# Optimization experiments

Hardware: AMD Instinct MI355X
Metric: run time of the kernel (lower is better)

Reference implementation:

```python
import jax, jax.numpy as jnp
import numpy as np

B, S, T, D_IN = 32, 64, 30, 500  # batch, outer seq, LSTM time steps, LSTM input size
L = 64  # stacked LSTM layers, hidden_size = 1


def setup_inputs() -> dict:
    key = jax.random.key(0)
    ks = jax.random.split(key, 9)
    s = 0.2  # param scale ~ uniform(-1,1) stddev regime of torch init (1/sqrt(hidden)=1)
    return {
        "x": jax.random.normal(ks[0], (B, S, T * D_IN), jnp.float32),
        "w_ih0": jax.random.normal(ks[1], (4, D_IN), jnp.float32) * s,
        "w_hh0": jax.random.normal(ks[2], (4, 1), jnp.float32) * s,
        "b_ih0": jax.random.normal(ks[3], (4,), jnp.float32) * s,
        "b_hh0": jax.random.normal(ks[4], (4,), jnp.float32) * s,
        "w_ih": jax.random.normal(ks[5], (L - 1, 4, 1), jnp.float32) * s,
        "w_hh": jax.random.normal(ks[6], (L - 1, 4, 1), jnp.float32) * s,
        "b_ih": jax.random.normal(ks[7], (L - 1, 4), jnp.float32) * s,
        "b_hh": jax.random.normal(ks[8], (L - 1, 4), jnp.float32) * s,
    }


def _scan_layer(pre, whh):
    """Run one hidden-width-1 LSTM layer. pre: (T, N, 4) input-side gate preacts
    (incl. both biases); whh: (4,) recurrent weights. Returns hidden stream (T, N)."""
    N = pre.shape[1]
    z = jnp.zeros((N,), pre.dtype)

    def cell(carry, g_in):
        h, c = carry
        g = g_in + h[:, None] * whh  # (N, 4), torch gate order i,f,g,o
        i = jax.nn.sigmoid(g[:, 0])
        f = jax.nn.sigmoid(g[:, 1])
        gg = jnp.tanh(g[:, 2])
        o = jax.nn.sigmoid(g[:, 3])
        c = f * c + i * gg
        h = o * jnp.tanh(c)
        return (h, c), h

    _, hs = jax.lax.scan(cell, (z, z), pre)
    return hs  # (T, N)


def reference(x, w_ih0, w_hh0, b_ih0, b_hh0, w_ih, w_hh, b_ih, b_hh):
    b, s, d = x.shape
    xf = jnp.flip(x, -1).reshape(b * s, T, D_IN)  # (N, T, 500)
    # layer 0: precompute input contribution for all timesteps (the only GEMM)
    pre0 = jnp.einsum('ntd,gd->tng', xf, w_ih0) + b_ih0 + b_hh0  # (T, N, 4)
    hs = _scan_layer(pre0, w_hh0[:, 0])  # (T, N)

    # layers 1..63: scalar-input LSTMs, scanned over the layer axis
    def layer_step(seq, params):
        wih, whh, bias = params  # (4,), (4,), (4,)
        pre = seq[:, :, None] * wih + bias  # (T, N, 4)
        return _scan_layer(pre, whh), None

    hs, _ = jax.lax.scan(layer_step, hs, (w_ih[:, :, 0], w_hh[:, :, 0], b_ih + b_hh))
    return hs.transpose(1, 0).reshape(b, s, T)  # (B, S, 30)
```

## Files before the change

### kernel.cpp

```cpp
#include <hip/hip_runtime.h>

#define NSEQ 2048
#define TT 30
#define DIN 500
#define NLAYER 64

__device__ __forceinline__ float fexp(float x) {
    return __builtin_amdgcn_exp2f(x * 1.4426950408889634f);
}
__device__ __forceinline__ float fsigmoid(float x) {
    return __builtin_amdgcn_rcpf(1.0f + fexp(-x));
}
__device__ __forceinline__ float ftanh_(float x) {
    return fmaf(-2.0f, __builtin_amdgcn_rcpf(1.0f + fexp(2.0f * x)), 1.0f);
}
__device__ __forceinline__ float rdlane(float v, int l) {
    return __builtin_bit_cast(float, __builtin_amdgcn_readlane(__builtin_bit_cast(int, v), l));
}
template <int CTRL>
__device__ __forceinline__ float dppmv(float v) {
    return __builtin_bit_cast(float, __builtin_amdgcn_update_dpp(
        0, __builtin_bit_cast(int, v), CTRL, 0xF, 0xF, false));
}
#define DPP_XOR1 0xB1
#define DPP_XOR2 0x4E
#define DPP_ROR4 0x124
#define DPP_ROR8 0x128
#define DPP_SHR1 0x138

__device__ __forceinline__ float dot4rev(const float4 xv, const float4 wv, float acc) {
    acc = fmaf(xv.x, wv.w, acc);
    acc = fmaf(xv.y, wv.z, acc);
    acc = fmaf(xv.z, wv.y, acc);
    acc = fmaf(xv.w, wv.x, acc);
    return acc;
}

__global__ __launch_bounds__(256, 2) void fused_lstm(
    const float* __restrict__ x,
    const float* __restrict__ w_ih0,
    const float* __restrict__ w_hh0,
    const float* __restrict__ b_ih0,
    const float* __restrict__ b_hh0,
    const float* __restrict__ w_ih,
    const float* __restrict__ w_hh,
    const float* __restrict__ b_ih,
    const float* __restrict__ b_hh,
    float* __restrict__ out)
{
    __shared__ float pre[4][TT * 4];

    const int tid  = threadIdx.x;
    const int lane = tid & 63;
    const int w    = tid >> 6;
    const int n    = blockIdx.x * 4 + w;
    const int s    = lane & 15;
    const int g    = lane >> 4;
    float* __restrict__ prew = pre[w];

    const float4* __restrict__ w4 = (const float4*)w_ih0;
    const float4 z4 = make_float4(0.f, 0.f, 0.f, 0.f);
    float4 wk[8];
#pragma unroll
    for (int k = 0; k < 8; ++k) {
        const int j = k * 16 + s;
        wk[k] = (j < 125) ? w4[g * 125 + (124 - j)] : z4;
    }

    const float4* __restrict__ xq = (const float4*)(x + (size_t)n * (TT * DIN));
    auto xload = [&](int t, float4 (&b)[8]) {
        const float4* __restrict__ p = xq + (TT - 1 - t) * 125;
#pragma unroll
        for (int k = 0; k < 8; ++k) {
            const int j = k * 16 + s;
            b[k] = p[(j < 125) ? j : 124];
        }
    };
    auto compute = [&](const float4 (&b)[8], int t) {
        float a = 0.f;
#pragma unroll
        for (int k = 0; k < 8; ++k) a = dot4rev(b[k], wk[k], a);
        a += dppmv<DPP_XOR1>(a);
        a += dppmv<DPP_XOR2>(a);
        a += dppmv<DPP_ROR4>(a);
        a += dppmv<DPP_ROR8>(a);
        if (s == 0) prew[t * 4 + g] = a;
    };

    float4 A[8], B[8];
    xload(0, A);
#pragma unroll
    for (int t = 0; t < TT; t += 2) {
        xload(t + 1, B);
        compute(A, t);
        if (t + 2 < TT) xload(t + 2, A);
        compute(B, t + 1);
    }
    asm volatile("s_waitcnt lgkmcnt(0)" ::: "memory");

    float wih0 = 0.f, wih1 = 0.f, wih2 = 0.f, wih3 = 0.f;
    float whh0, whh1, whh2, whh3;
    float bia0 = 0.f, bia1 = 0.f, bia2 = 0.f, bia3 = 0.f;
    if (lane == 0) {
        whh0 = w_hh0[0]; whh1 = w_hh0[1]; whh2 = w_hh0[2]; whh3 = w_hh0[3];
    } else {
        const int l = lane - 1;
        wih0 = w_ih[l * 4 + 0]; wih1 = w_ih[l * 4 + 1];
        wih2 = w_ih[l * 4 + 2]; wih3 = w_ih[l * 4 + 3];
        whh0 = w_hh[l * 4 + 0]; whh1 = w_hh[l * 4 + 1];
        whh2 = w_hh[l * 4 + 2]; whh3 = w_hh[l * 4 + 3];
        bia0 = b_ih[l * 4 + 0] + b_hh[l * 4 + 0];
        bia1 = b_ih[l * 4 + 1] + b_hh[l * 4 + 1];
        bia2 = b_ih[l * 4 + 2] + b_hh[l * 4 + 2];
        bia3 = b_ih[l * 4 + 3] + b_hh[l * 4 + 3];
    }
    float pg0 = 0.f, pg1 = 0.f, pg2 = 0.f, pg3 = 0.f;
    if (lane < TT) {
        const float4 q = *(const float4*)&prew[lane * 4];
        pg0 = q.x + b_ih0[0] + b_hh0[0];
        pg1 = q.y + b_ih0[1] + b_hh0[1];
        pg2 = q.z + b_ih0[2] + b_hh0[2];
        pg3 = q.w + b_ih0[3] + b_hh0[3];
    }

    float h = 0.f, c = 0.f;
    for (int k = 0; k < NLAYER + TT - 1; ++k) {
        const float h_in = dppmv<DPP_SHR1>(h);
        const int t = k - lane;
        const bool active = (t >= 0) && (t < TT);

        float g0, g1, g2, g3;
        if (lane == 0) {
            g0 = g1 = g2 = g3 = 0.f;
        } else {
            g0 = fmaf(h_in, wih0, bia0);
            g1 = fmaf(h_in, wih1, bia1);
            g2 = fmaf(h_in, wih2, bia2);
            g3 = fmaf(h_in, wih3, bia3);
        }
        if (k < TT) {
            const float p0 = rdlane(pg0, k);
            const float p1 = rdlane(pg1, k);
            const float p2 = rdlane(pg2, k);
            const float p3 = rdlane(pg3, k);
            if (lane == 0) { g0 = p0; g1 = p1; g2 = p2; g3 = p3; }
        }
        g0 = fmaf(h, whh0, g0);
        g1 = fmaf(h, whh1, g1);
        g2 = fmaf(h, whh2, g2);
        g3 = fmaf(h, whh3, g3);

        const float ig = fsigmoid(g0);
        const float fg = fsigmoid(g1);
        const float gg = ftanh_(g2);
        const float og = fsigmoid(g3);
        const float cn = fmaf(fg, c, ig * gg);
        const float hn = og * ftanh_(cn);

        if (active) { c = cn; h = hn; }
        if (lane == 63 && active) out[(size_t)n * TT + t] = hn;
    }
}

extern "C" void kernel_launch(void* const* d_in, const int* in_sizes, int n_in,
                              void* d_out, int out_size, void* d_ws, size_t ws_size,
                              hipStream_t stream) {
    const float* x     = (const float*)d_in[0];
    const float* w_ih0 = (const float*)d_in[1];
    const float* w_hh0 = (const float*)d_in[2];
    const float* b_ih0 = (const float*)d_in[3];
    const float* b_hh0 = (const float*)d_in[4];
    const float* w_ih  = (const float*)d_in[5];
    const float* w_hh  = (const float*)d_in[6];
    const float* b_ih  = (const float*)d_in[7];
    const float* b_hh  = (const float*)d_in[8];
    float* out = (float*)d_out;

    fused_lstm<<<NSEQ / 4, 256, 0, stream>>>(x, w_ih0, w_hh0, b_ih0, b_hh0,
                                             w_ih, w_hh, b_ih, b_hh, out);
}
```

Baseline: 42.80 us.

## Compute all four gates per lane group over distinct timesteps to reuse x loads

Reorganizes the layer-0 input projection so each 16-lane group processes a different timestep and accumulates all four gate dot products, loading each x row once per wave instead of once per gate group. All w_ih0 gate weights are held in registers. Small parameter loads are also vectorized and hoisted before the GEMM. This raises register pressure substantially and wastes two timestep slots in the final round.

Measured after the change: 42.11 us. Within noise of the previous version (-1.6%).

```diff
diff --git a/kernel.cpp b/kernel.cpp
--- a/kernel.cpp
+++ b/kernel.cpp
@@ -34,6 +34,13 @@
     acc = fmaf(xv.z, wv.y, acc);
     acc = fmaf(xv.w, wv.x, acc);
     return acc;
+}
+__device__ __forceinline__ float red16(float a) {
+    a += dppmv<DPP_XOR1>(a);
+    a += dppmv<DPP_XOR2>(a);
+    a += dppmv<DPP_ROR4>(a);
+    a += dppmv<DPP_ROR8>(a);
+    return a;
 }
 
 __global__ __launch_bounds__(256, 2) void fused_lstm(
@@ -58,69 +65,86 @@
     const int g    = lane >> 4;
     float* __restrict__ prew = pre[w];
 
+    const int l = (lane == 0) ? 0 : (lane - 1);
+    float4 wihv  = *(const float4*)(w_ih + l * 4);
+    float4 whhv  = *(const float4*)(w_hh + l * 4);
+    float4 bihv  = *(const float4*)(b_ih + l * 4);
+    float4 bhhv  = *(const float4*)(b_hh + l * 4);
+    float4 whh0v = *(const float4*)(w_hh0);
+    float4 bi0v  = *(const float4*)(b_ih0);
+    float4 bh0v  = *(const float4*)(b_hh0);
+    __builtin_amdgcn_sched_barrier(0);
+
     const float4* __restrict__ w4 = (const float4*)w_ih0;
     const float4 z4 = make_float4(0.f, 0.f, 0.f, 0.f);
-    float4 wk[8];
-#pragma unroll
-    for (int k = 0; k < 8; ++k) {
-        const int j = k * 16 + s;
-        wk[k] = (j < 125) ? w4[g * 125 + (124 - j)] : z4;
+    float4 wk[4][8];
+#pragma unroll
+    for (int gate = 0; gate < 4; ++gate) {
+#pragma unroll
+        for (int k = 0; k < 8; ++k) {
+            const int j = k * 16 + s;
+            wk[gate][k] = (j < 125) ? w4[gate * 125 + (124 - j)] : z4;
+        }
     }
 
     const float4* __restrict__ xq = (const float4*)(x + (size_t)n * (TT * DIN));
-    auto xload = [&](int t, float4 (&b)[8]) {
-        const float4* __restrict__ p = xq + (TT - 1 - t) * 125;
+    auto xround = [&](int r, float4 (&b)[8]) {
+        const int t = r * 4 + g;
+        int cc = TT - 1 - t; if (cc < 0) cc = 0;
+        const float4* __restrict__ p = xq + cc * 125;
 #pragma unroll
         for (int k = 0; k < 8; ++k) {
             const int j = k * 16 + s;
             b[k] = p[(j < 125) ? j : 124];
         }
     };
-    auto compute = [&](const float4 (&b)[8], int t) {
-        float a = 0.f;
-#pragma unroll
-        for (int k = 0; k < 8; ++k) a = dot4rev(b[k], wk[k], a);
-        a += dppmv<DPP_XOR1>(a);
-        a += dppmv<DPP_XOR2>(a);
-        a += dppmv<DPP_ROR4>(a);
-        a += dppmv<DPP_ROR8>(a);
-        if (s == 0) prew[t * 4 + g] = a;
+    auto cround = [&](const float4 (&b)[8], int r) {
+        float a0 = 0.f, a1 = 0.f, a2 = 0.f, a3 = 0.f;
+#pragma unroll
+        for (int k = 0; k < 8; ++k) {
+            a0 = dot4rev(b[k], wk[0][k], a0);
+            a1 = dot4rev(b[k], wk[1][k], a1);
+            a2 = dot4rev(b[k], wk[2][k], a2);
+            a3 = dot4rev(b[k], wk[3][k], a3);
+        }
+        a0 = red16(a0); a1 = red16(a1); a2 = red16(a2); a3 = red16(a3);
+        const int t = r * 4 + g;
+        if (s == 0 && t < TT)
+            *(float4*)&prew[t * 4] = make_float4(a0, a1, a2, a3);
     };
 
     float4 A[8], B[8];
-    xload(0, A);
-#pragma unroll
-    for (int t = 0; t < TT; t += 2) {
-        xload(t + 1, B);
-        compute(A, t);
-        if (t + 2 < TT) xload(t + 2, A);
-        compute(B, t + 1);
+    xround(0, A);
+#pragma unroll
+    for (int r = 0; r < 8; r += 2) {
+        if (r + 1 < 8) xround(r + 1, B);
+        __builtin_amdgcn_sched_barrier(0);
+        cround(A, r);
+        if (r + 2 < 8) xround(r + 2, A);
+        __builtin_amdgcn_sched_barrier(0);
+        cround(B, r + 1);
     }
     asm volatile("s_waitcnt lgkmcnt(0)" ::: "memory");
 
-    float wih0 = 0.f, wih1 = 0.f, wih2 = 0.f, wih3 = 0.f;
-    float whh0, whh1, whh2, whh3;
-    float bia0 = 0.f, bia1 = 0.f, bia2 = 0.f, bia3 = 0.f;
+    float wih0, wih1, wih2, wih3, whh0, whh1, whh2, whh3;
+    float bia0, bia1, bia2, bia3;
     if (lane == 0) {
-        whh0 = w_hh0[0]; whh1 = w_hh0[1]; whh2 = w_hh0[2]; whh3 = w_hh0[3];
+        wih0 = wih1 = wih2 = wih3 = 0.f;
+        bia0 = bia1 = bia2 = bia3 = 0.f;
+        whh0 = whh0v.x; whh1 = whh0v.y; whh2 = whh0v.z; whh3 = whh0v.w;
     } else {
-        const int l = lane - 1;
-        wih0 = w_ih[l * 4 + 0]; wih1 = w_ih[l * 4 + 1];
-        wih2 = w_ih[l * 4 + 2]; wih3 = w_ih[l * 4 + 3];
-        whh0 = w_hh[l * 4 + 0]; whh1 = w_hh[l * 4 + 1];
-        whh2 = w_hh[l * 4 + 2]; whh3 = w_hh[l * 4 + 3];
-        bia0 = b_ih[l * 4 + 0] + b_hh[l * 4 + 0];
-        bia1 = b_ih[l * 4 + 1] + b_hh[l * 4 + 1];
-        bia2 = b_ih[l * 4 + 2] + b_hh[l * 4 + 2];
-        bia3 = b_ih[l * 4 + 3] + b_hh[l * 4 + 3];
+        wih0 = wihv.x; wih1 = wihv.y; wih2 = wihv.z; wih3 = wihv.w;
+        whh0 = whhv.x; whh1 = whhv.y; whh2 = whhv.z; whh3 = whhv.w;
+        bia0 = bihv.x + bhhv.x; bia1 = bihv.y + bhhv.y;
+        bia2 = bihv.z + bhhv.z; bia3 = bihv.w + bhhv.w;
     }
     float pg0 = 0.f, pg1 = 0.f, pg2 = 0.f, pg3 = 0.f;
     if (lane < TT) {
         const float4 q = *(const float4*)&prew[lane * 4];
-        pg0 = q.x + b_ih0[0] + b_hh0[0];
-        pg1 = q.y + b_ih0[1] + b_hh0[1];
-        pg2 = q.z + b_ih0[2] + b_hh0[2];
-        pg3 = q.w + b_ih0[3] + b_hh0[3];
+        pg0 = q.x + bi0v.x + bh0v.x;
+        pg1 = q.y + bi0v.y + bh0v.y;
+        pg2 = q.z + bi0v.z + bh0v.z;
+        pg3 = q.w + bi0v.w + bh0v.w;
     }
 
     float h = 0.f, c = 0.f;
```
